# Optimization experiments

Hardware: AMD Instinct MI355X
Metric: run time of the kernel (lower is better)

The kernel has to match this reference:

```python
import jax, jax.numpy as jnp
import numpy as np

B, C, H, W = 4, 512, 64, 64
RED = 2
IC = C // RED  # inter_channels = 256


def _conv1x1(x, w, b):
    # mmcv ConvModule default: conv(+bias) then ReLU
    return jax.nn.relu(jnp.einsum('bchw,oc->bohw', x, w) + b[None, :, None, None])


def setup_inputs() -> dict:
    key = jax.random.key(0)
    ks = jax.random.split(key, 9)
    s_q = 0.02  # small init so exp(-dist) stays in a sane range
    return {
        'features': jax.random.normal(ks[0], (B, C, H, W), jnp.float32),
        'qw': jax.random.normal(ks[1], (IC, C), jnp.float32) * s_q,
        'qb': jnp.zeros((IC,), jnp.float32),
        'kw': jax.random.normal(ks[2], (IC, C), jnp.float32) * s_q,
        'kb': jnp.zeros((IC,), jnp.float32),
        'vw': jax.random.normal(ks[3], (C, C), jnp.float32) * s_q,
        'vb': jnp.zeros((C,), jnp.float32),
        'cw': jax.random.normal(ks[4], (IC, 2), jnp.float32) * s_q,
        'cb': jnp.zeros((IC,), jnp.float32),
    }


def reference(features, qw, qb, kw, kb, vw, vb, cw, cb):
    b, c, h, w = features.shape
    q = _conv1x1(features, qw, qb)   # [b, IC, h, w]
    k = _conv1x1(features, kw, kb)   # [b, IC, h, w]
    v = _conv1x1(features, vw, vb)   # [b, C,  h, w]

    # coordinate grid: channel 0 varies along w, channel 1 along h
    lin = jnp.linspace(-1.0, 1.0, h)
    A = jnp.broadcast_to(lin[None, :], (h, w))
    coord = jnp.broadcast_to(jnp.stack([A, A.T], axis=0)[None], (b, 2, h, w))
    cc = _conv1x1(coord, cw, cb)     # [b, IC, h, w]

    q = q + cc
    k = k + cc

    n = h * w
    Qf = q.reshape(b, -1, n).transpose(0, 2, 1)  # [b, n, IC]
    Kf = k.reshape(b, -1, n)                     # [b, IC, n]

    dots = jnp.einsum('bnc,bcm->bnm', Qf, Kf)    # [b, n, n]
    a_sq = jnp.sum(Qf * Qf, axis=-1)             # [b, n]
    b_sq = jnp.sum(Kf * Kf, axis=1)              # [b, n]
    D = a_sq[:, :, None] + b_sq[:, None, :] - 2.0 * dots
    S = jnp.exp(-D)
    S = S / (jnp.sum(S, axis=-1, keepdims=True) + 1e-14)

    Vf = v.reshape(b, c, n)                      # [b, C, n]
    out = jnp.einsum('bcn,bnm->bcm', Vf, S).reshape(b, c, h, w)
    return out + features
```

## Files before the change

### kernel.cpp

```cpp
#include <hip/hip_runtime.h>
#include <math.h>

#define BATCH 4
#define CH    512
#define ICH   256
#define NPIX  4096

typedef short short8 __attribute__((ext_vector_type(8)));
typedef float floatx4 __attribute__((ext_vector_type(4)));

#define BK   64
#define TS   136

static __device__ __forceinline__ unsigned short f2bf(float x) {
    union { float f; unsigned u; } v; v.f = x;
    unsigned r = (v.u + 0x7FFF + ((v.u >> 16) & 1)) >> 16;
    return (unsigned short)r;
}
static __device__ __forceinline__ float bf2f(unsigned short u) {
    union { unsigned u; float f; } v; v.u = ((unsigned)u) << 16; return v.f;
}
static __device__ __forceinline__ unsigned pack_bf(unsigned ue, unsigned uo) {
    return ((ue + 0x8000u) >> 16) | ((uo + 0x8000u) & 0xFFFF0000u);
}

static __device__ __forceinline__ void gld16(const unsigned short* g, unsigned short* l) {
    __builtin_amdgcn_global_load_lds(
        (const __attribute__((address_space(1))) unsigned int*)g,
        (__attribute__((address_space(3))) unsigned int*)l,
        16, 0, 0);
}

#define STAGE_TILE(L, M, row0, RS, k0)                                        \
    {                                                                         \
        int r_  = (it*32) + wid*8 + (lane >> 3);                              \
        int c_  = (lane & 7) ^ ((lane >> 3) & 7);                             \
        gld16(&(M)[(size_t)((row0) + r_)*(RS) + (k0) + c_*8],                 \
              &(L)[(it*32 + wid*8)*64]);                                      \
    }

#define STG64(L, M, row0, RS, k0, u)                                          \
    {                                                                         \
        int r_  = (u)*64 + wid*8 + (lane >> 3);                               \
        int c_  = (lane & 7) ^ ((lane >> 3) & 7);                             \
        gld16(&(M)[(size_t)((row0) + r_)*(RS) + (k0) + c_*8],                 \
              &(L)[((u)*64 + wid*8)*64]);                                     \
    }

#define FRAG(L, row, ks) \
    (*(const short8*)&(L)[(row)*64 + (((((ks)<<2) + quad) ^ (lo & 7)) << 3)])

__global__ __launch_bounds__(256)
void prep_w(const float* __restrict__ qw, const float* __restrict__ kw,
            const float* __restrict__ vw, unsigned short* __restrict__ Wb)
{
    int i = (blockIdx.x*256 + threadIdx.x) * 4;
    const float* src;
    int off;
    if (i < 256*512)            { src = qw; off = i; }
    else if (i < 512*512)       { src = kw; off = i - 256*512; }
    else                        { src = vw; off = i - 512*512; }
    float4 f = *(const float4*)&src[off];
    unsigned short pk[4] = { f2bf(f.x), f2bf(f.y), f2bf(f.z), f2bf(f.w) };
    *(uint2*)&Wb[i] = *(uint2*)pk;
}

__global__ __launch_bounds__(256)
void prep_ft(const float* __restrict__ feat, unsigned short* __restrict__ Ft)
{
    __shared__ unsigned short S[64][65];
    const int t = threadIdx.x;
    const int n0 = blockIdx.x * 64, c0 = blockIdx.y * 64, b = blockIdx.z;

    #pragma unroll
    for (int rep = 0; rep < 4; rep++) {
        int cl = rep*16 + (t >> 4), col4 = (t & 15) * 4;
        float4 f = *(const float4*)&feat[((size_t)b*CH + c0 + cl)*NPIX + n0 + col4];
        S[cl][col4 + 0] = f2bf(f.x);
        S[cl][col4 + 1] = f2bf(f.y);
        S[cl][col4 + 2] = f2bf(f.z);
        S[cl][col4 + 3] = f2bf(f.w);
    }
    __syncthreads();
    #pragma unroll
    for (int rep = 0; rep < 4; rep++) {
        int nn = rep*16 + (t >> 4), cq = t & 15;
        unsigned short h4[4];
        #pragma unroll
        for (int j = 0; j < 4; j++) h4[j] = S[cq*4 + j][nn];
        *(uint2*)&Ft[((size_t)b*NPIX + n0 + nn)*CH + c0 + cq*4] = *(uint2*)h4;
    }
}

__global__ __launch_bounds__(256)
void conv_mfma(const unsigned short* __restrict__ Ft,
               const unsigned short* __restrict__ Wb,
               const float* __restrict__ qb, const float* __restrict__ kb,
               const float* __restrict__ vb,
               const float* __restrict__ cw, const float* __restrict__ cb,
               unsigned short* __restrict__ Qt, unsigned short* __restrict__ Kt,
               unsigned short* __restrict__ Vt)
{
    __shared__ unsigned short SH[128*TS];
    unsigned short* L0 = SH;
    unsigned short* L2 = SH + 128*64;

    const int tid = threadIdx.x;
    const int wid = tid >> 6, lane = tid & 63, quad = lane >> 4, lo = lane & 15;
    const int n0 = blockIdx.x * 128;
    const int yb = blockIdx.y;
    const int bz = blockIdx.z;
    const int o_base = yb * 128;
    const int waveA = (wid >> 1) * 64, waveB = (wid & 1) * 64;
    const int is_v = (yb >= 4);
    const size_t fb = (size_t)bz*NPIX;

    floatx4 acc[4][4] = {};

    for (int k0 = 0; k0 < CH; k0 += BK) {
        #pragma unroll
        for (int it = 0; it < 4; it++) {
            STAGE_TILE(L0, Ft, fb + n0, CH, k0);
            STAGE_TILE(L2, Wb, o_base,  CH, k0);
        }
        __syncthreads();
        if (!is_v) {
            #pragma unroll
            for (int ks = 0; ks < 2; ks++) {
                short8 af[4], bw[4];
                #pragma unroll
                for (int i = 0; i < 4; i++) af[i] = FRAG(L0, waveA + i*16 + lo, ks);
                #pragma unroll
                for (int j = 0; j < 4; j++) bw[j] = FRAG(L2, waveB + j*16 + lo, ks);
                #pragma unroll
                for (int i = 0; i < 4; i++)
                    #pragma unroll
                    for (int j = 0; j < 4; j++)
                        acc[i][j] = __builtin_amdgcn_mfma_f32_16x16x32_bf16(af[i], bw[j], acc[i][j], 0, 0, 0);
            }
        } else {
            #pragma unroll
            for (int ks = 0; ks < 2; ks++) {
                short8 aw[4], bf[4];
                #pragma unroll
                for (int i = 0; i < 4; i++) aw[i] = FRAG(L2, waveA + i*16 + lo, ks);
                #pragma unroll
                for (int j = 0; j < 4; j++) bf[j] = FRAG(L0, waveB + j*16 + lo, ks);
                #pragma unroll
                for (int i = 0; i < 4; i++)
                    #pragma unroll
                    for (int j = 0; j < 4; j++)
                        acc[i][j] = __builtin_amdgcn_mfma_f32_16x16x32_bf16(aw[i], bf[j], acc[i][j], 0, 0, 0);
            }
        }
        __syncthreads();
    }

    const float step = 2.0f / 63.0f;
    if (!is_v) {
        const float* bp = (yb < 2) ? qb : kb;
        const int icg0 = (yb & 1) * 128;
        #pragma unroll
        for (int ib = 0; ib < 4; ib++) {
            int colL = waveB + ib*16 + lo;
            int ic = icg0 + colL;
            float bias = bp[ic];
            float cw0 = cw[ic*2+0], cw1 = cw[ic*2+1], cbv = cb[ic];
            #pragma unroll
            for (int ia = 0; ia < 4; ia++) {
                int rowL = waveA + ia*16 + quad*4;
                #pragma unroll
                for (int r = 0; r < 4; r++) {
                    int n = n0 + rowL + r;
                    float cx = -1.f + (n & 63)*step;
                    float cy = -1.f + (n >> 6)*step;
                    float v = fmaxf(acc[ia][ib][r] + bias, 0.f)
                            + fmaxf(cw0*cx + cw1*cy + cbv, 0.f);
                    unsigned u = __float_as_uint(v);
                    unsigned p = __shfl_xor(u, 1, 64);
                    if ((lo & 1) == 0)
                        *(unsigned*)&SH[(rowL + r)*TS + colL] = pack_bf(u, p);
                }
            }
        }
    } else {
        const int c_blk0 = (yb - 4) * 128;
        #pragma unroll
        for (int ia = 0; ia < 4; ia++) {
            int rowL = waveA + ia*16 + quad*4;
            #pragma unroll
            for (int r = 0; r < 4; r++) {
                float bias = vb[c_blk0 + rowL + r];
                #pragma unroll
                for (int ib = 0; ib < 4; ib++) {
                    int colL = waveB + ib*16 + lo;
                    float v = fmaxf(acc[ia][ib][r] + bias, 0.f);
                    unsigned u = __float_as_uint(v);
                    unsigned p = __shfl_xor(u, 1, 64);
                    if ((lo & 1) == 0)
                        *(unsigned*)&SH[(rowL + r)*TS + colL] = pack_bf(u, p);
                }
            }
        }
    }
    __syncthreads();

    unsigned short* dstp;
    int row0, rs, col0;
    if (!is_v) { dstp = ((yb < 2) ? Qt : Kt) + (size_t)bz*NPIX*ICH;
                 row0 = n0; rs = ICH; col0 = (yb & 1) * 128; }
    else       { dstp = Vt + (size_t)bz*CH*NPIX;
                 row0 = (yb - 4) * 128; rs = NPIX; col0 = n0; }
    #pragma unroll
    for (int it = 0; it < 8; it++) {
        int f = it*256 + tid;
        int row = f >> 4, col = (f & 15) * 8;
        uint4 v = *(const uint4*)&SH[row*TS + col];
        *(uint4*)&dstp[(size_t)(row0 + row)*rs + col0 + col] = v;
    }
}

__global__ __launch_bounds__(256)
void sqb_kernel(const unsigned short* __restrict__ Qt,
                const unsigned short* __restrict__ Kt,
                float* __restrict__ asq, float* __restrict__ bsq)
{
    int n = blockIdx.x*256 + threadIdx.x;
    int b = blockIdx.y;
    const unsigned short* q = Qt + ((size_t)b*NPIX + n)*ICH;
    const unsigned short* k = Kt + ((size_t)b*NPIX + n)*ICH;
    float qs = 0.f, ks = 0.f;
    #pragma unroll 4
    for (int i = 0; i < ICH/8; i++) {
        uint4 v = *(const uint4*)&q[i*8];
        const unsigned short* s = (const unsigned short*)&v;
        #pragma unroll
        for (int j = 0; j < 8; j++) { float a = bf2f(s[j]); qs += a*a; }
        uint4 w = *(const uint4*)&k[i*8];
        const unsigned short* t = (const unsigned short*)&w;
        #pragma unroll
        for (int j = 0; j < 8; j++) { float a = bf2f(t[j]); ks += a*a; }
    }
    asq[b*NPIX + n] = qs;
    bsq[b*NPIX + n] = ks;
}

__global__ __launch_bounds__(512)
void dots_mfma(const unsigned short* __restrict__ Kt_,
               const unsigned short* __restrict__ Qt_,
               const float* __restrict__ asq_, const float* __restrict__ bsq_,
               unsigned short* __restrict__ St_, float* __restrict__ rsum_,
               int b0)
{
    __shared__ unsigned short SH[128*TS];
    unsigned short* Al = SH;
    unsigned short* Bl = SH + 8192;

    const int tid = threadIdx.x;
    const int wid = tid >> 6, lane = tid & 63, quad = lane >> 4, lo = lane & 15;
    const int wm = wid >> 2;
    const int wn = wid & 3;
    const int m0 = blockIdx.x * 128, n0 = blockIdx.y * 128;
    const int bz = blockIdx.z, gb = b0 + bz;

    const unsigned short* Kt = Kt_ + (size_t)gb*NPIX*ICH;
    const unsigned short* Qt = Qt_ + (size_t)gb*NPIX*ICH;
    const float* asq = asq_ + (size_t)gb*NPIX;
    const float* bsq = bsq_ + (size_t)gb*NPIX;
    unsigned short* St = St_ + (size_t)bz*NPIX*NPIX;
    float* rsum = rsum_ + (size_t)gb*NPIX;

    floatx4 acc[4][2] = {};

    for (int k0 = 0; k0 < ICH; k0 += BK) {
        STG64(Al, Kt, m0, ICH, k0, 0);
        STG64(Al, Kt, m0, ICH, k0, 1);
        STG64(Bl, Qt, n0, ICH, k0, 0);
        STG64(Bl, Qt, n0, ICH, k0, 1);
        __syncthreads();
        #pragma unroll
        for (int ks = 0; ks < 2; ks++) {
            short8 a[4], bfr[2];
            #pragma unroll
            for (int i = 0; i < 4; i++) a[i]  = FRAG(Al, wm*64 + i*16 + lo, ks);
            #pragma unroll
            for (int j = 0; j < 2; j++) bfr[j] = FRAG(Bl, wn*32 + j*16 + lo, ks);
            #pragma unroll
            for (int i = 0; i < 4; i++)
                #pragma unroll
                for (int j = 0; j < 2; j++)
                    acc[i][j] = __builtin_amdgcn_mfma_f32_16x16x32_bf16(
                        a[i], bfr[j], acc[i][j], 0, 0, 0);
        }
        __syncthreads();
    }

    #pragma unroll
    for (int j = 0; j < 2; j++) {
        int nl = wn*32 + j*16 + lo;
        float aq = asq[n0 + nl];
        float colsum = 0.f;
        #pragma unroll
        for (int i = 0; i < 4; i++) {
            int mb = wm*64 + i*16 + quad*4;
            #pragma unroll
            for (int r = 0; r < 4; r++) {
                float d = aq + bsq[m0 + mb + r] - 2.f*acc[i][j][r];
                float sv = __expf(-d);
                colsum += sv;
                unsigned u = __float_as_uint(sv);
                unsigned p = __shfl_xor(u, 1, 64);
                if ((lo & 1) == 0)
                    *(unsigned*)&SH[(mb + r)*TS + nl] = pack_bf(u, p);
            }
        }
        colsum += __shfl_xor(colsum, 16, 64);
        colsum += __shfl_xor(colsum, 32, 64);
        if (quad == 0) atomicAdd(&rsum[n0 + nl], colsum);
    }
    __syncthreads();

    #pragma unroll
    for (int it = 0; it < 4; it++) {
        int f = it*512 + tid;
        int row = f >> 4, col = (f & 15) * 8;
        uint4 v = *(const uint4*)&SH[row*TS + col];
        *(uint4*)&St[(size_t)(m0 + row)*NPIX + n0 + col] = v;
    }
}

__global__ __launch_bounds__(256)
void vscale_kernel(const unsigned short* __restrict__ Vt,
                   const float* __restrict__ rsum,
                   unsigned short* __restrict__ Vp, int b0)
{
    int gb = b0 + blockIdx.y;
    size_t base = (size_t)gb*CH*NPIX + ((size_t)blockIdx.x*256 + threadIdx.x) * 8;
    int n = (int)(base & (NPIX - 1));
    const float* rs = rsum + (size_t)gb*NPIX;
    uint4 v = *(const uint4*)&Vt[base];
    const unsigned short* s = (const unsigned short*)&v;
    unsigned short pk[8];
    #pragma unroll
    for (int i = 0; i < 8; i++)
        pk[i] = f2bf(bf2f(s[i]) / (rs[n + i] + 1e-14f));
    *(uint4*)&Vp[base] = *(uint4*)pk;
}

#define PVBUF 24576
#define PVNT  (NPIX/BK)

__global__ __launch_bounds__(512)
void pv_mfma(const unsigned short* __restrict__ Vp_,
             const unsigned short* __restrict__ St_,
             const float* __restrict__ feat_, float* __restrict__ out_,
             int b0)
{
    __shared__ unsigned short SH3[3*PVBUF];
    const int tid = threadIdx.x;
    const int wid = tid >> 6, lane = tid & 63, quad = lane >> 4, lo = lane & 15;
    const int wm = wid >> 2;
    const int wn = wid & 3;
    const int m0 = blockIdx.x * 256, c0 = blockIdx.y * 128;
    const int bz = blockIdx.z, gb = b0 + bz;

    const unsigned short* Vp = Vp_ + (size_t)gb*CH*NPIX;
    const unsigned short* St = St_ + (size_t)bz*NPIX*NPIX;
    const float* feat = feat_ + (size_t)gb*CH*NPIX;
    float* out = out_ + (size_t)gb*CH*NPIX;

    floatx4 acc[4][4] = {};

    {
        unsigned short* A0 = SH3;            unsigned short* B0 = SH3 + 128*64;
        unsigned short* A1 = SH3 + PVBUF;    unsigned short* B1 = A1  + 128*64;
        STG64(A0, Vp, c0, NPIX, 0, 0);  STG64(A0, Vp, c0, NPIX, 0, 1);
        STG64(B0, St, m0, NPIX, 0, 0);  STG64(B0, St, m0, NPIX, 0, 1);
        STG64(B0, St, m0, NPIX, 0, 2);  STG64(B0, St, m0, NPIX, 0, 3);
        STG64(A1, Vp, c0, NPIX, BK, 0); STG64(A1, Vp, c0, NPIX, BK, 1);
        STG64(B1, St, m0, NPIX, BK, 0); STG64(B1, St, m0, NPIX, BK, 1);
        STG64(B1, St, m0, NPIX, BK, 2); STG64(B1, St, m0, NPIX, BK, 3);
    }
    asm volatile("s_waitcnt vmcnt(6)" ::: "memory");
    __builtin_amdgcn_s_barrier();

    int pc = 0, pn = 2;
    for (int s = 0; s < PVNT; ++s) {
        unsigned short* Ac = SH3 + pc*PVBUF;
        unsigned short* Bc = Ac + 128*64;
        unsigned short* An = SH3 + pn*PVBUF;
        unsigned short* Bn = An + 128*64;
        const int k2 = (s + 2) * BK;
        const bool stg = (s < PVNT - 2);

        short8 a0[2][4], b0[2][4];
        #pragma unroll
        for (int ks = 0; ks < 2; ks++) {
            #pragma unroll
            for (int i = 0; i < 4; i++)
                a0[ks][i] = FRAG(Ac, wm*64 + i*16 + lo, ks);
            #pragma unroll
            for (int j = 0; j < 4; j++)
                b0[ks][j] = FRAG(Bc, wn*64 + j*16 + lo, ks);
        }
        if (stg) {
            STG64(An, Vp, c0, NPIX, k2, 0);
            STG64(An, Vp, c0, NPIX, k2, 1);
            STG64(Bn, St, m0, NPIX, k2, 0);
            STG64(Bn, St, m0, NPIX, k2, 1);
            STG64(Bn, St, m0, NPIX, k2, 2);
            STG64(Bn, St, m0, NPIX, k2, 3);
        }
        __builtin_amdgcn_s_setprio(1);
        #pragma unroll
        for (int ks = 0; ks < 2; ks++)
            #pragma unroll
            for (int i = 0; i < 4; i++)
                #pragma unroll
                for (int j = 0; j < 4; j++)
                    acc[i][j] = __builtin_amdgcn_mfma_f32_16x16x32_bf16(
                        a0[ks][i], b0[ks][j], acc[i][j], 0, 0, 0);
        __builtin_amdgcn_s_setprio(0);

        if (stg)                asm volatile("s_waitcnt vmcnt(6)" ::: "memory");
        else if (s == PVNT - 2) asm volatile("s_waitcnt vmcnt(0)" ::: "memory");
        __builtin_amdgcn_s_barrier();

        pc = (pc == 2) ? 0 : pc + 1;
        pn = (pn == 2) ? 0 : pn + 1;
    }

    #pragma unroll
    for (int i = 0; i < 4; i++) {
        int cr = c0 + wm*64 + i*16 + quad*4;
        #pragma unroll
        for (int r = 0; r < 4; r++) {
            size_t rowbase = (size_t)(cr + r)*NPIX;
            #pragma unroll
            for (int j = 0; j < 4; j++) {
                int m = m0 + wn*64 + j*16 + lo;
                out[rowbase + m] = acc[i][j][r] + feat[rowbase + m];
            }
        }
    }
}

extern "C" void kernel_launch(void* const* d_in, const int* in_sizes, int n_in,
                              void* d_out, int out_size, void* d_ws, size_t ws_size,
                              hipStream_t stream)
{
    const float* feat = (const float*)d_in[0];
    const float* qw   = (const float*)d_in[1];
    const float* qb   = (const float*)d_in[2];
    const float* kw   = (const float*)d_in[3];
    const float* kb   = (const float*)d_in[4];
    const float* vw   = (const float*)d_in[5];
    const float* vb   = (const float*)d_in[6];
    const float* cw   = (const float*)d_in[7];
    const float* cb   = (const float*)d_in[8];
    float* out = (float*)d_out;
    char* ws = (char*)d_ws;
    char* ws0 = ws;

    unsigned short* Ft  = (unsigned short*)ws;  ws += (size_t)BATCH*NPIX*CH*2;
    unsigned short* Wb  = (unsigned short*)ws;  ws += (size_t)1024*CH*2;
    unsigned short* Qt  = (unsigned short*)ws;  ws += (size_t)BATCH*NPIX*ICH*2;
    unsigned short* Kt  = (unsigned short*)ws;  ws += (size_t)BATCH*NPIX*ICH*2;
    unsigned short* Vt  = (unsigned short*)ws;  ws += (size_t)BATCH*CH*NPIX*2;
    unsigned short* Vp  = (unsigned short*)ws;  ws += (size_t)BATCH*CH*NPIX*2;
    float*         asq  = (float*)ws;           ws += (size_t)BATCH*NPIX*4;
    float*         bsq  = (float*)ws;           ws += (size_t)BATCH*NPIX*4;
    float*         rsum = (float*)ws;           ws += (size_t)BATCH*NPIX*4;
    unsigned short* St  = (unsigned short*)ws;

    const size_t st1 = (size_t)NPIX*NPIX*2;
    const size_t fixed = (size_t)(ws - ws0);
    const int nb = (ws_size >= fixed + (size_t)BATCH*st1) ? BATCH : 1;

    hipMemsetAsync(rsum, 0, (size_t)BATCH*NPIX*sizeof(float), stream);

    prep_w<<<dim3(512), 256, 0, stream>>>(qw, kw, vw, Wb);
    prep_ft<<<dim3(NPIX/64, CH/64, BATCH), 256, 0, stream>>>(feat, Ft);

    conv_mfma<<<dim3(NPIX/128, 8, BATCH), 256, 0, stream>>>(
        Ft, Wb, qb, kb, vb, cw, cb, Qt, Kt, Vt);

    sqb_kernel<<<dim3(NPIX/256, BATCH), 256, 0, stream>>>(Qt, Kt, asq, bsq);

    for (int b0 = 0; b0 < BATCH; b0 += nb) {
        dots_mfma<<<dim3(NPIX/128, NPIX/128, nb), 512, 0, stream>>>(
            Kt, Qt, asq, bsq, St, rsum, b0);
        vscale_kernel<<<dim3(CH*NPIX/(256*8), nb), 256, 0, stream>>>(
            Vt, rsum, Vp, b0);
        pv_mfma<<<dim3(NPIX/256, CH/128, nb), 512, 0, stream>>>(
            Vp, St, feat, out, b0);
    }
}
```

Baseline: 294.5 us.

## Use 512-thread conv blocks, exp2-based softmax epilogue, and reciprocal in vscale

The conv kernel now launches 8 waves per block instead of 4, so each wave computes a 64x32 sub-tile instead of 64x64 and tile staging uses the 64-row macro. The dots epilogue folds the distance computation into a single fma feeding exp2f, with the bsq values premultiplied by log2(e) and hoisted out of the column loop. vscale replaces its division with a hardware reciprocal. Together these aim to raise wave-level parallelism in the conv GEMM and cut ALU cost in the elementwise epilogues, in exchange for more waves per block and slightly lower precision in the normalization.

Result: faster. 271.6 us (-7.8%).

```diff
diff --git a/kernel.cpp b/kernel.cpp
--- a/kernel.cpp
+++ b/kernel.cpp
@@ -30,14 +30,6 @@
         (__attribute__((address_space(3))) unsigned int*)l,
         16, 0, 0);
 }
-
-#define STAGE_TILE(L, M, row0, RS, k0)                                        \
-    {                                                                         \
-        int r_  = (it*32) + wid*8 + (lane >> 3);                              \
-        int c_  = (lane & 7) ^ ((lane >> 3) & 7);                             \
-        gld16(&(M)[(size_t)((row0) + r_)*(RS) + (k0) + c_*8],                 \
-              &(L)[(it*32 + wid*8)*64]);                                      \
-    }
 
 #define STG64(L, M, row0, RS, k0, u)                                          \
     {                                                                         \
@@ -92,7 +84,7 @@
     }
 }
 
-__global__ __launch_bounds__(256)
+__global__ __launch_bounds__(512)
 void conv_mfma(const unsigned short* __restrict__ Ft,
                const unsigned short* __restrict__ Wb,
                const float* __restrict__ qb, const float* __restrict__ kb,
@@ -111,45 +103,45 @@
     const int yb = blockIdx.y;
     const int bz = blockIdx.z;
     const int o_base = yb * 128;
-    const int waveA = (wid >> 1) * 64, waveB = (wid & 1) * 64;
+    const int wm = wid >> 2;
+    const int wn = wid & 3;
     const int is_v = (yb >= 4);
     const size_t fb = (size_t)bz*NPIX;
 
-    floatx4 acc[4][4] = {};
+    floatx4 acc[4][2] = {};
 
     for (int k0 = 0; k0 < CH; k0 += BK) {
-        #pragma unroll
-        for (int it = 0; it < 4; it++) {
-            STAGE_TILE(L0, Ft, fb + n0, CH, k0);
-            STAGE_TILE(L2, Wb, o_base,  CH, k0);
-        }
+        STG64(L0, Ft, fb + n0, CH, k0, 0);
+        STG64(L0, Ft, fb + n0, CH, k0, 1);
+        STG64(L2, Wb, o_base,  CH, k0, 0);
+        STG64(L2, Wb, o_base,  CH, k0, 1);
         __syncthreads();
         if (!is_v) {
             #pragma unroll
             for (int ks = 0; ks < 2; ks++) {
-                short8 af[4], bw[4];
-                #pragma unroll
-                for (int i = 0; i < 4; i++) af[i] = FRAG(L0, waveA + i*16 + lo, ks);
-                #pragma unroll
-                for (int j = 0; j < 4; j++) bw[j] = FRAG(L2, waveB + j*16 + lo, ks);
+                short8 af[4], bw[2];
+                #pragma unroll
+                for (int i = 0; i < 4; i++) af[i] = FRAG(L0, wm*64 + i*16 + lo, ks);
+                #pragma unroll
+                for (int j = 0; j < 2; j++) bw[j] = FRAG(L2, wn*32 + j*16 + lo, ks);
                 #pragma unroll
                 for (int i = 0; i < 4; i++)
                     #pragma unroll
-                    for (int j = 0; j < 4; j++)
+                    for (int j = 0; j < 2; j++)
                         acc[i][j] = __builtin_amdgcn_mfma_f32_16x16x32_bf16(af[i], bw[j], acc[i][j], 0, 0, 0);
             }
         } else {
             #pragma unroll
             for (int ks = 0; ks < 2; ks++) {
-                short8 aw[4], bf[4];
-                #pragma unroll
-                for (int i = 0; i < 4; i++) aw[i] = FRAG(L2, waveA + i*16 + lo, ks);
-                #pragma unroll
-                for (int j = 0; j < 4; j++) bf[j] = FRAG(L0, waveB + j*16 + lo, ks);
+                short8 aw[4], bf[2];
+                #pragma unroll
+                for (int i = 0; i < 4; i++) aw[i] = FRAG(L2, wm*64 + i*16 + lo, ks);
+                #pragma unroll
+                for (int j = 0; j < 2; j++) bf[j] = FRAG(L0, wn*32 + j*16 + lo, ks);
                 #pragma unroll
                 for (int i = 0; i < 4; i++)
                     #pragma unroll
-                    for (int j = 0; j < 4; j++)
+                    for (int j = 0; j < 2; j++)
                         acc[i][j] = __builtin_amdgcn_mfma_f32_16x16x32_bf16(aw[i], bf[j], acc[i][j], 0, 0, 0);
             }
         }
@@ -161,14 +153,14 @@
         const float* bp = (yb < 2) ? qb : kb;
         const int icg0 = (yb & 1) * 128;
         #pragma unroll
-        for (int ib = 0; ib < 4; ib++) {
-            int colL = waveB + ib*16 + lo;
+        for (int ib = 0; ib < 2; ib++) {
+            int colL = wn*32 + ib*16 + lo;
             int ic = icg0 + colL;
             float bias = bp[ic];
             float cw0 = cw[ic*2+0], cw1 = cw[ic*2+1], cbv = cb[ic];
             #pragma unroll
             for (int ia = 0; ia < 4; ia++) {
-                int rowL = waveA + ia*16 + quad*4;
+                int rowL = wm*64 + ia*16 + quad*4;
                 #pragma unroll
                 for (int r = 0; r < 4; r++) {
                     int n = n0 + rowL + r;
@@ -187,13 +179,13 @@
         const int c_blk0 = (yb - 4) * 128;
         #pragma unroll
         for (int ia = 0; ia < 4; ia++) {
-            int rowL = waveA + ia*16 + quad*4;
+            int rowL = wm*64 + ia*16 + quad*4;
             #pragma unroll
             for (int r = 0; r < 4; r++) {
                 float bias = vb[c_blk0 + rowL + r];
                 #pragma unroll
-                for (int ib = 0; ib < 4; ib++) {
-                    int colL = waveB + ib*16 + lo;
+                for (int ib = 0; ib < 2; ib++) {
+                    int colL = wn*32 + ib*16 + lo;
                     float v = fmaxf(acc[ia][ib][r] + bias, 0.f);
                     unsigned u = __float_as_uint(v);
                     unsigned p = __shfl_xor(u, 1, 64);
@@ -212,8 +204,8 @@
     else       { dstp = Vt + (size_t)bz*CH*NPIX;
                  row0 = (yb - 4) * 128; rs = NPIX; col0 = n0; }
     #pragma unroll
-    for (int it = 0; it < 8; it++) {
-        int f = it*256 + tid;
+    for (int it = 0; it < 4; it++) {
+        int f = it*512 + tid;
         int row = f >> 4, col = (f & 15) * 8;
         uint4 v = *(const uint4*)&SH[row*TS + col];
         *(uint4*)&dstp[(size_t)(row0 + row)*rs + col0 + col] = v;
@@ -295,18 +287,26 @@
         __syncthreads();
     }
 
+    const float L2E  = 1.44269504f;
+    const float L2E2 = 2.88539008f;
+    float bL[4][4];
+    #pragma unroll
+    for (int i = 0; i < 4; i++) {
+        int mb = wm*64 + i*16 + quad*4;
+        #pragma unroll
+        for (int r = 0; r < 4; r++) bL[i][r] = bsq[m0 + mb + r] * L2E;
+    }
     #pragma unroll
     for (int j = 0; j < 2; j++) {
         int nl = wn*32 + j*16 + lo;
-        float aq = asq[n0 + nl];
+        float aqL = asq[n0 + nl] * L2E;
         float colsum = 0.f;
         #pragma unroll
         for (int i = 0; i < 4; i++) {
             int mb = wm*64 + i*16 + quad*4;
             #pragma unroll
             for (int r = 0; r < 4; r++) {
-                float d = aq + bsq[m0 + mb + r] - 2.f*acc[i][j][r];
-                float sv = __expf(-d);
+                float sv = exp2f(fmaf(acc[i][j][r], L2E2, -(aqL + bL[i][r])));
                 colsum += sv;
                 unsigned u = __float_as_uint(sv);
                 unsigned p = __shfl_xor(u, 1, 64);
@@ -343,7 +343,7 @@
     unsigned short pk[8];
     #pragma unroll
     for (int i = 0; i < 8; i++)
-        pk[i] = f2bf(bf2f(s[i]) / (rs[n + i] + 1e-14f));
+        pk[i] = f2bf(bf2f(s[i]) * __builtin_amdgcn_rcpf(rs[n + i] + 1e-14f));
     *(uint4*)&Vp[base] = *(uint4*)pk;
 }
 
@@ -482,7 +482,7 @@
     prep_w<<<dim3(512), 256, 0, stream>>>(qw, kw, vw, Wb);
     prep_ft<<<dim3(NPIX/64, CH/64, BATCH), 256, 0, stream>>>(feat, Ft);
 
-    conv_mfma<<<dim3(NPIX/128, 8, BATCH), 256, 0, stream>>>(
+    conv_mfma<<<dim3(NPIX/128, 8, BATCH), 512, 0, stream>>>(
         Ft, Wb, qb, kb, vb, cw, cb, Qt, Kt, Vt);
 
     sqb_kernel<<<dim3(NPIX/256, BATCH), 256, 0, stream>>>(Qt, Kt, asq, bsq);
```
